# Optimization experiments

Hardware: AMD Instinct MI355X
Metric: run time of the kernel (lower is better)

## Reference

```python
import jax, jax.numpy as jnp
import numpy as np

B, S, DIM = 2, 1024, 2048
H, NOPE, ROPE_D, VD = 16, 128, 64, 128
QKD = NOPE + ROPE_D  # 192
BASE = 10000
NEG_INF = -1e9


def _rope_cos_sin(seq_len, start_pos=0):
    # theta: [ROPE_D//2]
    theta = 1.0 / (BASE ** (jnp.arange(0, ROPE_D, 2, dtype=jnp.float32) / ROPE_D))
    pos = jnp.arange(start_pos, start_pos + seq_len, dtype=jnp.float32)
    ang = pos[:, None] * theta[None, :]  # [s, ROPE_D//2]
    return jnp.cos(ang), jnp.sin(ang)


def _apply_rope(x, cos, sin):
    # x: [b, s, h, d]; cos/sin: [s, d//2]
    b, s, h, d = x.shape
    xs = x.astype(jnp.float32).reshape(b, s, h, d // 2, 2)
    c = cos[None, :, None, :]
    sn = sin[None, :, None, :]
    out = jnp.stack([xs[..., 0] * c - xs[..., 1] * sn,
                     xs[..., 1] * c + xs[..., 0] * sn], axis=-1)
    return out.reshape(b, s, h, d).astype(x.dtype)


def setup_inputs() -> dict:
    key = jax.random.key(0)
    ks = jax.random.split(key, 6)
    x = jax.random.normal(ks[0], (B, S, DIM), dtype=jnp.float32)
    sc = lambda fan_in: 1.0 / np.sqrt(fan_in)
    Wq = jax.random.normal(ks[1], (DIM, H * QKD), dtype=jnp.float32) * sc(DIM)
    Wk = jax.random.normal(ks[2], (DIM, H * QKD), dtype=jnp.float32) * sc(DIM)
    Wv = jax.random.normal(ks[3], (DIM, H * VD), dtype=jnp.float32) * sc(DIM)
    Wo = jax.random.normal(ks[4], (H * VD, DIM), dtype=jnp.float32) * sc(H * VD)
    bo = jnp.zeros((DIM,), dtype=jnp.float32)
    mask = jnp.where(jnp.tril(jnp.ones((S, S), dtype=bool)), 0.0, NEG_INF).astype(jnp.float32)
    return {"x": x, "Wq": Wq, "Wk": Wk, "Wv": Wv, "Wo": Wo, "bo": bo,
            "mask": mask, "start_pos": 0}


def reference(x, Wq, Wk, Wv, Wo, bo, mask, start_pos):
    b, s, _ = x.shape
    q = (x @ Wq).reshape(b, s, H, QKD)
    k = (x @ Wk).reshape(b, s, H, QKD)
    v = (x @ Wv).reshape(b, s, H, VD)
    q_nope, q_rope = q[..., :NOPE], q[..., NOPE:]
    k_nope, k_rope = k[..., :NOPE], k[..., NOPE:]
    cos, sin = _rope_cos_sin(s)  # input_pos=None -> positions 0..s-1
    q_rope = _apply_rope(q_rope, cos, sin)
    k_rope = _apply_rope(k_rope, cos, sin)
    q = jnp.concatenate([q_nope, q_rope], axis=-1)
    k = jnp.concatenate([k_nope, k_rope], axis=-1)
    # start_pos=0 prefill: cache[:end_pos] == k, v just written
    scale = QKD ** -0.5
    scores = jnp.einsum('bshd,bthd->bsht', q, k) * scale
    scores = scores + mask[:, None, :]  # mask.unsqueeze(1) on [b,s,h,t] broadcasting
    weights = jax.nn.softmax(scores.astype(jnp.float32), axis=-1).astype(x.dtype)
    c_v = jnp.einsum('bsht,bthd->bshd', weights, v)
    return c_v.reshape(b, s, H * VD) @ Wo + bo
```

## Files before the change

### kernel.cpp

```cpp
#include <hip/hip_runtime.h>


typedef __bf16 bf16;
typedef __bf16 bf16x8 __attribute__((ext_vector_type(8)));
typedef __bf16 bf16x4 __attribute__((ext_vector_type(4)));
typedef float  f32x4  __attribute__((ext_vector_type(4)));

#define DEVI __device__ __forceinline__

static constexpr int Bc = 2, Sc = 1024, DIMc = 2048, Hc = 16;
static constexpr int NOPEc = 128, QKDc = 192, VDc = 128;
static constexpr int NQ    = Hc * QKDc;
static constexpr int NCAT  = NQ + NQ + Hc*VDc;

__global__ __launch_bounds__(256) void k_prep(const float* __restrict__ x,
                                              const float* __restrict__ Wq, const float* __restrict__ Wk,
                                              const float* __restrict__ Wv, const float* __restrict__ Wo,
                                              bf16* __restrict__ xb, bf16* __restrict__ wcat,
                                              bf16* __restrict__ woT,
                                              float* __restrict__ cosT, float* __restrict__ sinT) {
    __shared__ float tile[64][68];
    const int yt = blockIdx.y, xt = blockIdx.x, tid = threadIdx.x;
    if (yt < 160) {
        const float* src; bf16* dst; int N, n0;
        if (yt < 48)       { src = Wq; N = 3072; n0 = yt * 64;         dst = wcat; }
        else if (yt < 96)  { src = Wk; N = 3072; n0 = (yt - 48) * 64;  dst = wcat + (size_t)3072 * 2048; }
        else if (yt < 128) { src = Wv; N = 2048; n0 = (yt - 96) * 64;  dst = wcat + (size_t)6144 * 2048; }
        else               { src = Wo; N = 2048; n0 = (yt - 128) * 64; dst = woT; }
        int k0 = xt * 64;
        int tr = tid >> 4, tc = (tid & 15) * 4;
#pragma unroll
        for (int i = 0; i < 4; i++) {
            int r = tr + i * 16;
            float4 v = *(const float4*)(src + (size_t)(k0 + r) * N + n0 + tc);
            tile[r][tc+0] = v.x; tile[r][tc+1] = v.y; tile[r][tc+2] = v.z; tile[r][tc+3] = v.w;
        }
        __syncthreads();
#pragma unroll
        for (int i = 0; i < 4; i++) {
            int n = tr + i * 16;
            bf16x4 o;
#pragma unroll
            for (int j = 0; j < 4; j++) o[j] = (bf16)tile[tc + j][n];
            *(bf16x4*)(dst + (size_t)(n0 + n) * 2048 + k0 + tc) = o;
        }
    } else if (yt < 224) {
        int i = (((yt - 160) * 32 + xt) * 256 + tid) * 8;
        float4 a = *(const float4*)(x + i);
        float4 b = *(const float4*)(x + i + 4);
        bf16x8 o;
        o[0]=(bf16)a.x; o[1]=(bf16)a.y; o[2]=(bf16)a.z; o[3]=(bf16)a.w;
        o[4]=(bf16)b.x; o[5]=(bf16)b.y; o[6]=(bf16)b.z; o[7]=(bf16)b.w;
        *(bf16x8*)(xb + i) = o;
    } else {
#pragma unroll
        for (int p = 0; p < 4; p++) {
            int idx = p * 8192 + xt * 256 + tid;
            int pos = idx >> 5, i = idx & 31;
            float theta = expf(-(float)i * (9.210340371976184f / 32.0f));
            float ang = (float)pos * theta;
            cosT[idx] = cosf(ang);
            sinT[idx] = sinf(ang);
        }
    }
}

__global__ __launch_bounds__(256) void k_rope2(bf16* __restrict__ qkv, const float* __restrict__ cosT,
                                               const float* __restrict__ sinT) {
    int bidx = blockIdx.x;
    int secbase = (bidx >= 1024) ? NQ : 0;
    int idx = (bidx & 1023) * 256 + threadIdx.x;
    int g = idx & 7, h = (idx >> 3) & 15, row = idx >> 7;
    int s = row & (Sc - 1);
    bf16* p = qkv + (size_t)row * NCAT + secbase + h * QKDc + NOPEc + g * 8;
    bf16x8 v = *(bf16x8*)p;
    const float* cp = cosT + s * 32 + g * 4;
    const float* sp = sinT + s * 32 + g * 4;
#pragma unroll
    for (int q = 0; q < 4; q++) {
        float x0 = (float)v[2*q], x1 = (float)v[2*q+1];
        float c = cp[q], sn = sp[q];
        v[2*q]   = (bf16)(x0 * c - x1 * sn);
        v[2*q+1] = (bf16)(x1 * c + x0 * sn);
    }
    *(bf16x8*)p = v;
}

__global__ __launch_bounds__(256) void k_vt(const bf16* __restrict__ qkv, bf16* __restrict__ vT) {
    int st = blockIdx.x, dt = blockIdx.y, bh = blockIdx.z;
    int b = bh >> 4, h = bh & 15;
    __shared__ bf16 tile[64][72];
    int r = threadIdx.x >> 3, c8 = (threadIdx.x & 7) * 8;
    const bf16* src = qkv + (size_t)(b * Sc + st * 64) * NCAT + 2 * NQ + h * VDc + dt * 64;
#pragma unroll
    for (int i = 0; i < 2; i++) {
        int rr = r + i * 32;
        *(bf16x8*)&tile[rr][c8] = *(const bf16x8*)(src + (size_t)rr * NCAT + c8);
    }
    __syncthreads();
    bf16* dst = vT + ((size_t)bh * 128 + dt * 64) * Sc + st * 64;
#pragma unroll
    for (int i = 0; i < 2; i++) {
        int rr = r + i * 32;
        bf16x8 o;
#pragma unroll
        for (int j = 0; j < 8; j++) o[j] = tile[c8 + j][rr];
        *(bf16x8*)(dst + (size_t)rr * Sc + c8) = o;
    }
}

DEVI void gload16(const bf16* g, bf16* l) {
    __builtin_amdgcn_global_load_lds((const __attribute__((address_space(1))) void*)g,
                                     (__attribute__((address_space(3))) void*)l, 16, 0, 0);
}

__global__ __launch_bounds__(512, 2) void k_gemm8(const bf16* __restrict__ A, const bf16* __restrict__ Bt,
                                                  bf16* __restrict__ C, int N, int K, int NCT) {
    __shared__ __align__(16) bf16 lds[2][2][2][256 * 32];
    const int tid = threadIdx.x;
    const int l = tid & 63, wid = tid >> 6;
    const int lg = l >> 4, lc = l & 15;
    const int wm = wid >> 2, wn = wid & 3;
    const int bid = blockIdx.x;
    const int xcd = bid & 7, g = bid >> 3;
    const int per = NCT >> 3;
    const int rt = g & 7, ct = xcd * per + (g >> 3);
    const int row0 = rt * 256, col0 = ct * 256;
    const int NT = K >> 6;

    const bf16* Abase = A  + (size_t)row0 * K;
    const bf16* Bbase = Bt + (size_t)col0 * K;

    size_t srcoff0, srcoff1;
    int ldsoff0, ldsoff1;
    {
        int li0 = tid,        r0 = li0 >> 2, u0 = li0 & 3;
        int li1 = 512 + tid,  r1 = li1 >> 2, u1 = li1 & 3;
        srcoff0 = (size_t)r0 * K + ((u0 ^ ((r0 >> 1) & 3)) << 3);  ldsoff0 = li0 * 8;
        srcoff1 = (size_t)r1 * K + ((u1 ^ ((r1 >> 1) & 3)) << 3);  ldsoff1 = li1 * 8;
    }

#define STAGE8(ab, ks, ktile, buf) { \
    const bf16* gb_ = ((ab) ? Bbase : Abase) + (ktile) * 64 + (ks) * 32; \
    bf16* lb_ = &lds[buf][ab][ks][0]; \
    gload16(gb_ + srcoff0, lb_ + ldsoff0); \
    gload16(gb_ + srcoff1, lb_ + ldsoff1); }

#define RD_A(dst, P, hf) { _Pragma("unroll") \
    for (int i_ = 0; i_ < 4; i_++) { \
        int row_ = wm * 128 + ((hf) * 4 + i_) * 16 + lc; \
        dst[i_] = *(const bf16x8*)((P) + row_ * 32 + ((lg ^ ((row_ >> 1) & 3)) << 3)); } }
#define RD_B(dst, P) { _Pragma("unroll") \
    for (int fc_ = 0; fc_ < 4; fc_++) { \
        int row_ = wn * 64 + fc_ * 16 + lc; \
        dst[fc_] = *(const bf16x8*)((P) + row_ * 32 + ((lg ^ ((row_ >> 1) & 3)) << 3)); } }
#define MM(Av, Bv, mo) { _Pragma("unroll") \
    for (int i_ = 0; i_ < 4; i_++) _Pragma("unroll") \
        for (int fc_ = 0; fc_ < 4; fc_++) \
            acc[(mo) + i_][fc_] = __builtin_amdgcn_mfma_f32_16x16x32_bf16(Av[i_], Bv[fc_], acc[(mo) + i_][fc_], 0, 0, 0); }
#define BAR() { __builtin_amdgcn_s_barrier(); asm volatile("" ::: "memory"); }

    f32x4 acc[8][4] = {};

    STAGE8(0, 0, 0, 0); STAGE8(1, 0, 0, 0); STAGE8(0, 1, 0, 0); STAGE8(1, 1, 0, 0);
    asm volatile("s_waitcnt vmcnt(4)" ::: "memory");
    BAR();

    for (int kt = 0; kt < NT; ++kt) {
        const int cur = kt & 1, nxt = cur ^ 1;
        const bool notlast = (kt + 1 < NT);
        const bf16* A0_ = &lds[cur][0][0][0];
        const bf16* A1_ = &lds[cur][0][1][0];
        const bf16* B0_ = &lds[cur][1][0][0];
        const bf16* B1_ = &lds[cur][1][1][0];
        bf16x8 aX[4], aY[4], bX[4], bY[4];
        RD_A(aX, A0_, 0);
        RD_B(bX, B0_);
        if (notlast) STAGE8(0, 0, kt + 1, nxt);
        RD_A(aY, A0_, 1);
        BAR();
        __builtin_amdgcn_s_setprio(1);
        MM(aX, bX, 0);
        __builtin_amdgcn_s_setprio(0);
        if (notlast) asm volatile("s_waitcnt vmcnt(2)" ::: "memory");
        else         asm volatile("s_waitcnt vmcnt(0)" ::: "memory");
        BAR();
        if (notlast) STAGE8(1, 0, kt + 1, nxt);
        RD_A(aX, A1_, 0);
        RD_B(bY, B1_);
        BAR();
        __builtin_amdgcn_s_setprio(1);
        MM(aY, bX, 4);
        __builtin_amdgcn_s_setprio(0);
        BAR();
        if (notlast) STAGE8(0, 1, kt + 1, nxt);
        RD_A(aY, A1_, 1);
        BAR();
        __builtin_amdgcn_s_setprio(1);
        MM(aX, bY, 0);
        __builtin_amdgcn_s_setprio(0);
        BAR();
        if (notlast) STAGE8(1, 1, kt + 1, nxt);
        BAR();
        __builtin_amdgcn_s_setprio(1);
        MM(aY, bY, 4);
        __builtin_amdgcn_s_setprio(0);
        if (notlast) asm volatile("s_waitcnt vmcnt(4)" ::: "memory");
        BAR();
    }
#undef STAGE8
#undef RD_A
#undef RD_B
#undef MM
#undef BAR
#pragma unroll
    for (int m = 0; m < 8; m++)
#pragma unroll
        for (int fc = 0; fc < 4; fc++)
#pragma unroll
            for (int j = 0; j < 4; j++) {
                int r = row0 + wm * 128 + m * 16 + lg * 4 + j;
                int c = col0 + wn * 64 + fc * 16 + lc;
                C[(size_t)r * N + c] = (bf16)acc[m][fc][j];
            }
}

__global__ __launch_bounds__(512, 2) void k_gemmO(const bf16* __restrict__ A, const bf16* __restrict__ Bt,
                                                  float* __restrict__ C, const float* __restrict__ bias,
                                                  int N, int K) {
    __shared__ __align__(16) bf16 lds[2][2][2][128 * 32];
    const int tid = threadIdx.x;
    const int l = tid & 63, wid = tid >> 6;
    const int lg = l >> 4, lc = l & 15;
    const int wm = wid >> 2, wn = wid & 3;
    const int bid = blockIdx.x;
    const int xcd = bid & 7, g = bid >> 3;
    const int rt = g & 15, ct = xcd * 2 + (g >> 4);
    const int row0 = rt * 128, col0 = ct * 128;
    const int NT = K >> 6;

    const bf16* Abase = A  + (size_t)row0 * K;
    const bf16* Bbase = Bt + (size_t)col0 * K;

    size_t srcoff; int ldsoff;
    {
        int r0 = tid >> 2, u0 = tid & 3;
        srcoff = (size_t)r0 * K + ((u0 ^ ((r0 >> 1) & 3)) << 3);
        ldsoff = tid * 8;
    }

#define STAGEO(ab, ks, ktile, buf) { \
    const bf16* gb_ = ((ab) ? Bbase : Abase) + (ktile) * 64 + (ks) * 32; \
    gload16(gb_ + srcoff, &lds[buf][ab][ks][0] + ldsoff); }

    f32x4 acc[4][2] = {};

    STAGEO(0, 0, 0, 0); STAGEO(1, 0, 0, 0); STAGEO(0, 1, 0, 0); STAGEO(1, 1, 0, 0);
    asm volatile("s_waitcnt vmcnt(2)" ::: "memory");
    __builtin_amdgcn_s_barrier();
    asm volatile("" ::: "memory");

    for (int kt = 0; kt < NT; ++kt) {
        const int cur = kt & 1, nxt = cur ^ 1;
        const bool notlast = (kt + 1 < NT);
#pragma unroll
        for (int ph = 0; ph < 2; ph++) {
            const bf16* As_ = &lds[cur][0][ph][0];
            const bf16* Bs_ = &lds[cur][1][ph][0];
            bf16x8 aF[4], bB[2];
#pragma unroll
            for (int n = 0; n < 2; n++) {
                int row = wn * 32 + n * 16 + lc;
                bB[n] = *(const bf16x8*)(Bs_ + row * 32 + ((lg ^ ((row >> 1) & 3)) << 3));
            }
#pragma unroll
            for (int m = 0; m < 4; m++) {
                int row = wm * 64 + m * 16 + lc;
                aF[m] = *(const bf16x8*)(As_ + row * 32 + ((lg ^ ((row >> 1) & 3)) << 3));
            }
            if (notlast) {
                if (ph == 0) { STAGEO(0, 0, kt + 1, nxt); STAGEO(1, 0, kt + 1, nxt); }
                else         { STAGEO(0, 1, kt + 1, nxt); STAGEO(1, 1, kt + 1, nxt); }
            }
            __builtin_amdgcn_s_barrier();
            asm volatile("" ::: "memory");
            __builtin_amdgcn_s_setprio(1);
#pragma unroll
            for (int m = 0; m < 4; m++)
#pragma unroll
                for (int n = 0; n < 2; n++)
                    acc[m][n] = __builtin_amdgcn_mfma_f32_16x16x32_bf16(aF[m], bB[n], acc[m][n], 0, 0, 0);
            __builtin_amdgcn_s_setprio(0);
            if (notlast)          asm volatile("s_waitcnt vmcnt(2)" ::: "memory");
            else if (ph == 0)     asm volatile("s_waitcnt vmcnt(0)" ::: "memory");
            __builtin_amdgcn_s_barrier();
            asm volatile("" ::: "memory");
        }
    }
#undef STAGEO
#pragma unroll
    for (int m = 0; m < 4; m++)
#pragma unroll
        for (int n = 0; n < 2; n++)
#pragma unroll
            for (int j = 0; j < 4; j++) {
                int r = row0 + wm * 64 + m * 16 + lg * 4 + j;
                int c = col0 + wn * 32 + n * 16 + lc;
                C[(size_t)r * N + c] = acc[m][n][j] + bias[c];
            }
}

__global__ __launch_bounds__(256, 3) void k_attn(const bf16* __restrict__ qkv, const bf16* __restrict__ vT,
                                                 bf16* __restrict__ cv) {
    const int bid = blockIdx.x;
    const int xcd = bid & 7, g = bid >> 3;
    const int qt = (g & 32) ? (g & 15) : (15 - (g & 15));
    const int bh = xcd + 8 * (g >> 4);
    const int b = bh >> 4, h = bh & 15;
    const int tid = threadIdx.x, l = tid & 63, w = tid >> 6;
    const int lg = l >> 4, lc = l & 15;
    __shared__ __align__(16) bf16 Ks[64 * 192];
    __shared__ __align__(16) bf16 Vs[128 * 64];
    __shared__ __align__(16) bf16 Pl[4][16][72];
    const bf16* Qb = qkv + (size_t)b * Sc * NCAT + h * QKDc;
    const bf16* Kb = Qb + NQ;
    const bf16* Vt = vT + (size_t)bh * 128 * Sc;

    int sK[6];
#pragma unroll
    for (int r = 0; r < 6; r++) {
        int li = r * 256 + tid;
        int row = li / 24, c16 = li - row * 24;
        sK[r] = row * NCAT + ((c16 ^ (row & 7)) * 8);
    }
    int sV[4];
#pragma unroll
    for (int r = 0; r < 4; r++) {
        int li = r * 256 + tid;
        int row = li >> 3, c16 = li & 7;
        sV[r] = row * Sc + ((c16 ^ (row & 7)) * 8);
    }
    const int swz = lc & 7;

    bf16x8 qF[6];
    const int qrow = qt * 64 + w * 16 + lc;
#pragma unroll
    for (int kc = 0; kc < 6; kc++) qF[kc] = *(const bf16x8*)(Qb + (size_t)qrow * NCAT + kc * 32 + lg * 8);

    f32x4 acc[8] = {};
    float mrow[4] = {-1e30f, -1e30f, -1e30f, -1e30f};
    float lsum[4] = {0.f, 0.f, 0.f, 0.f};
    const float scale = 0.07216878364870323f;

#pragma unroll
    for (int r = 0; r < 6; r++) gload16(Kb + sK[r], Ks + (r * 256 + tid) * 8);

    for (int c = 0; c <= qt; ++c) {
        const int t0 = c * 64;
        __syncthreads();
#pragma unroll
        for (int r = 0; r < 4; r++) gload16(Vt + t0 + sV[r], Vs + (r * 256 + tid) * 8);
        f32x4 sc[4] = {};
#pragma unroll
        for (int nt = 0; nt < 4; nt++)
#pragma unroll
            for (int kc = 0; kc < 6; kc++) {
                bf16x8 kf = *(const bf16x8*)(Ks + (nt * 16 + lc) * 192 + (((kc * 4 + lg) ^ swz) * 8));
                sc[nt] = __builtin_amdgcn_mfma_f32_16x16x32_bf16(qF[kc], kf, sc[nt], 0, 0, 0);
            }
        __syncthreads();
        if (c < qt) {
#pragma unroll
            for (int r = 0; r < 6; r++) gload16(Kb + (size_t)(t0 + 64) * NCAT + sK[r], Ks + (r * 256 + tid) * 8);
        }
        float p[4][4];
        float cmax[4] = {-1e30f, -1e30f, -1e30f, -1e30f};
        const bool diag = (c == qt);
#pragma unroll
        for (int nt = 0; nt < 4; nt++)
#pragma unroll
            for (int j = 0; j < 4; j++) {
                float v = sc[nt][j] * scale;
                if (diag) {
                    int tg = t0 + nt * 16 + lc;
                    int rg = qt * 64 + w * 16 + lg * 4 + j;
                    if (tg > rg) v = -1e9f;
                }
                p[nt][j] = v;
                cmax[j] = fmaxf(cmax[j], v);
            }
#pragma unroll
        for (int j = 0; j < 4; j++)
#pragma unroll
            for (int d = 1; d < 16; d <<= 1) cmax[j] = fmaxf(cmax[j], __shfl_xor(cmax[j], d));
        float f[4];
#pragma unroll
        for (int j = 0; j < 4; j++) {
            float nm = fmaxf(mrow[j], cmax[j]);
            f[j] = __expf(mrow[j] - nm);
            mrow[j] = nm;
        }
        float psum[4] = {0.f, 0.f, 0.f, 0.f};
#pragma unroll
        for (int nt = 0; nt < 4; nt++)
#pragma unroll
            for (int j = 0; j < 4; j++) {
                p[nt][j] = __expf(p[nt][j] - mrow[j]);
                psum[j] += p[nt][j];
            }
#pragma unroll
        for (int j = 0; j < 4; j++) {
#pragma unroll
            for (int d = 1; d < 16; d <<= 1) psum[j] += __shfl_xor(psum[j], d);
            lsum[j] = lsum[j] * f[j] + psum[j];
        }
#pragma unroll
        for (int n = 0; n < 8; n++)
#pragma unroll
            for (int j = 0; j < 4; j++) acc[n][j] *= f[j];
#pragma unroll
        for (int nt = 0; nt < 4; nt++)
#pragma unroll
            for (int j = 0; j < 4; j++)
                Pl[w][lg * 4 + j][nt * 16 + lc] = (bf16)p[nt][j];
#pragma unroll
        for (int ks = 0; ks < 2; ks++) {
            bf16x8 aP = *(const bf16x8*)(&Pl[w][lc][ks * 32 + lg * 8]);
#pragma unroll
            for (int n = 0; n < 8; n++) {
                bf16x8 bV = *(const bf16x8*)(Vs + (n * 16 + lc) * 64 + (((ks * 4 + lg) ^ swz) * 8));
                acc[n] = __builtin_amdgcn_mfma_f32_16x16x32_bf16(aP, bV, acc[n], 0, 0, 0);
            }
        }
    }
#pragma unroll
    for (int j = 0; j < 4; j++) {
        float inv = 1.0f / lsum[j];
        int r = qt * 64 + w * 16 + lg * 4 + j;
#pragma unroll
        for (int n = 0; n < 8; n++) {
            float v = acc[n][j] * inv;
            cv[((size_t)(b * Sc + r) * Hc + h) * VDc + n * 16 + lc] = (bf16)v;
        }
    }
}

extern "C" void kernel_launch(void* const* d_in, const int* in_sizes, int n_in,
                              void* d_out, int out_size, void* d_ws, size_t ws_size,
                              hipStream_t stream) {
    const float* x  = (const float*)d_in[0];
    const float* Wq = (const float*)d_in[1];
    const float* Wk = (const float*)d_in[2];
    const float* Wv = (const float*)d_in[3];
    const float* Wo = (const float*)d_in[4];
    const float* bo = (const float*)d_in[5];
    float* out = (float*)d_out;
    char* ws = (char*)d_ws;

    bf16*  wcat = (bf16*)(ws + 0);
    bf16*  woT  = (bf16*)(ws + 33554432);
    bf16*  xb   = (bf16*)(ws + 41943040);
    bf16*  qkvb = (bf16*)(ws + 50331648);
    bf16*  cvb  = (bf16*)(ws + 83886080);
    bf16*  vTb  = (bf16*)(ws + 92274688);
    float* cosT = (float*)(ws + 100663296);
    float* sinT = (float*)(ws + 100794368);

    k_prep<<<dim3(32, 225), 256, 0, stream>>>(x, Wq, Wk, Wv, Wo, xb, wcat, woT, cosT, sinT);
    k_gemm8<<<256, 512, 0, stream>>>(xb, wcat, qkvb, NCAT, DIMc, NCAT / 256);
    k_rope2<<<2048, 256, 0, stream>>>(qkvb, cosT, sinT);
    k_vt<<<dim3(16, 2, 32), 256, 0, stream>>>(qkvb, vTb);
    k_attn<<<512, 256, 0, stream>>>(qkvb, vTb, cvb);
    k_gemmO<<<256, 512, 0, stream>>>(cvb, woT, out, bo, DIMc, DIMc);
}
```

Baseline: 163.9 us.

## Simplify GEMM main loop to bulk prefetch with a single barrier per k-tile

Replaces the four-phase interleaved schedule (staggered stage loads, LDS reads and MFMA groups separated by many barriers) with a simpler loop. Each k-tile now issues all next-tile global-to-LDS loads up front, then computes both 32-wide k-halves with 8x4 MFMA blocks, then waits on vmcnt(0) and hits a single barrier. The aim is to cut barrier and waitcnt overhead per iteration. In exchange it loses the fine-grained overlap between LDS reads and MFMAs, and keeps more A fragments live at once, which raises register pressure.

```diff
diff --git a/kernel.cpp b/kernel.cpp
--- a/kernel.cpp
+++ b/kernel.cpp
@@ -146,72 +146,62 @@
     gload16(gb_ + srcoff0, lb_ + ldsoff0); \
     gload16(gb_ + srcoff1, lb_ + ldsoff1); }
 
-#define RD_A(dst, P, hf) { _Pragma("unroll") \
-    for (int i_ = 0; i_ < 4; i_++) { \
-        int row_ = wm * 128 + ((hf) * 4 + i_) * 16 + lc; \
+#define RD_A8(dst, P) { _Pragma("unroll") \
+    for (int i_ = 0; i_ < 8; i_++) { \
+        int row_ = wm * 128 + i_ * 16 + lc; \
         dst[i_] = *(const bf16x8*)((P) + row_ * 32 + ((lg ^ ((row_ >> 1) & 3)) << 3)); } }
-#define RD_B(dst, P) { _Pragma("unroll") \
+#define RD_B4(dst, P) { _Pragma("unroll") \
     for (int fc_ = 0; fc_ < 4; fc_++) { \
         int row_ = wn * 64 + fc_ * 16 + lc; \
         dst[fc_] = *(const bf16x8*)((P) + row_ * 32 + ((lg ^ ((row_ >> 1) & 3)) << 3)); } }
-#define MM(Av, Bv, mo) { _Pragma("unroll") \
-    for (int i_ = 0; i_ < 4; i_++) _Pragma("unroll") \
+#define MM32(Av, Bv) { _Pragma("unroll") \
+    for (int i_ = 0; i_ < 8; i_++) _Pragma("unroll") \
         for (int fc_ = 0; fc_ < 4; fc_++) \
-            acc[(mo) + i_][fc_] = __builtin_amdgcn_mfma_f32_16x16x32_bf16(Av[i_], Bv[fc_], acc[(mo) + i_][fc_], 0, 0, 0); }
+            acc[i_][fc_] = __builtin_amdgcn_mfma_f32_16x16x32_bf16(Av[i_], Bv[fc_], acc[i_][fc_], 0, 0, 0); }
 #define BAR() { __builtin_amdgcn_s_barrier(); asm volatile("" ::: "memory"); }
 
     f32x4 acc[8][4] = {};
 
     STAGE8(0, 0, 0, 0); STAGE8(1, 0, 0, 0); STAGE8(0, 1, 0, 0); STAGE8(1, 1, 0, 0);
-    asm volatile("s_waitcnt vmcnt(4)" ::: "memory");
+    asm volatile("s_waitcnt vmcnt(0)" ::: "memory");
     BAR();
 
     for (int kt = 0; kt < NT; ++kt) {
         const int cur = kt & 1, nxt = cur ^ 1;
         const bool notlast = (kt + 1 < NT);
-        const bf16* A0_ = &lds[cur][0][0][0];
-        const bf16* A1_ = &lds[cur][0][1][0];
-        const bf16* B0_ = &lds[cur][1][0][0];
-        const bf16* B1_ = &lds[cur][1][1][0];
-        bf16x8 aX[4], aY[4], bX[4], bY[4];
-        RD_A(aX, A0_, 0);
-        RD_B(bX, B0_);
-        if (notlast) STAGE8(0, 0, kt + 1, nxt);
-        RD_A(aY, A0_, 1);
-        BAR();
-        __builtin_amdgcn_s_setprio(1);
-        MM(aX, bX, 0);
-        __builtin_amdgcn_s_setprio(0);
-        if (notlast) asm volatile("s_waitcnt vmcnt(2)" ::: "memory");
-        else         asm volatile("s_waitcnt vmcnt(0)" ::: "memory");
-        BAR();
-        if (notlast) STAGE8(1, 0, kt + 1, nxt);
-        RD_A(aX, A1_, 0);
-        RD_B(bY, B1_);
-        BAR();
-        __builtin_amdgcn_s_setprio(1);
-        MM(aY, bX, 4);
-        __builtin_amdgcn_s_setprio(0);
-        BAR();
-        if (notlast) STAGE8(0, 1, kt + 1, nxt);
-        RD_A(aY, A1_, 1);
-        BAR();
-        __builtin_amdgcn_s_setprio(1);
-        MM(aX, bY, 0);
-        __builtin_amdgcn_s_setprio(0);
-        BAR();
-        if (notlast) STAGE8(1, 1, kt + 1, nxt);
-        BAR();
-        __builtin_amdgcn_s_setprio(1);
-        MM(aY, bY, 4);
-        __builtin_amdgcn_s_setprio(0);
-        if (notlast) asm volatile("s_waitcnt vmcnt(4)" ::: "memory");
-        BAR();
+        if (notlast) {
+            STAGE8(0, 0, kt + 1, nxt); STAGE8(1, 0, kt + 1, nxt);
+            STAGE8(0, 1, kt + 1, nxt); STAGE8(1, 1, kt + 1, nxt);
+        }
+        {
+            const bf16* A0_ = &lds[cur][0][0][0];
+            const bf16* B0_ = &lds[cur][1][0][0];
+            bf16x8 aF[8], bB[4];
+            RD_A8(aF, A0_);
+            RD_B4(bB, B0_);
+            __builtin_amdgcn_s_setprio(1);
+            MM32(aF, bB);
+            __builtin_amdgcn_s_setprio(0);
+        }
+        {
+            const bf16* A1_ = &lds[cur][0][1][0];
+            const bf16* B1_ = &lds[cur][1][1][0];
+            bf16x8 aF[8], bB[4];
+            RD_A8(aF, A1_);
+            RD_B4(bB, B1_);
+            __builtin_amdgcn_s_setprio(1);
+            MM32(aF, bB);
+            __builtin_amdgcn_s_setprio(0);
+        }
+        if (notlast) {
+            asm volatile("s_waitcnt vmcnt(0)" ::: "memory");
+            BAR();
+        }
     }
 #undef STAGE8
-#undef RD_A
-#undef RD_B
-#undef MM
+#undef RD_A8
+#undef RD_B4
+#undef MM32
 #undef BAR
 #pragma unroll
     for (int m = 0; m < 8; m++)
```

New measurement: 162.8 us. Within noise of the previous version (-0.7%).
